# Optimization experiments

Measured on AMD Instinct MI355X. Metric: run time of the kernel, lower is better.

Reference implementation:

```python
import jax, jax.numpy as jnp
import numpy as np

B, C, N, D, F = 2048, 64, 64, 64, 128  # batch, cin_hidden, num_features, embed_dim, feature_maps


def setup_inputs() -> dict:
    key = jax.random.key(0)
    k1, k2, k3 = jax.random.split(key, 3)
    xj = jax.random.normal(k1, (B, C, D), dtype=jnp.float32)
    x0 = jax.random.normal(k2, (B, N, D), dtype=jnp.float32)
    # xavier_uniform_ on (F, C, N): fan_in = C*N? torch treats dim1 as fan_in-ish;
    # exact init distribution is irrelevant for correctness testing, use scaled uniform.
    limit = float(np.sqrt(6.0 / (C + N)))
    W = jax.random.uniform(k3, (F, C, N), dtype=jnp.float32, minval=-limit, maxval=limit)
    return {"xj": xj, "x0": x0, "W": W}


def reference(xj, x0, W):
    # Original: hadamard[b,c,n,d] = x0[b,n,d]*xj[b,c,d];
    # out[b,f,c,d] = sum_n hadamard * W[f,c,n]; cin_out = sum_c out; cin_p_out = sum_d cin_out.
    # Fused: cin_out[b,f,d] = sum_{c,n} W[f,c,n] * xj[b,c,d] * x0[b,n,d]
    cin_out = jnp.einsum('bcd,bnd,fcn->bfd', xj, x0, W)  # (B, F, D)
    cin_p_out = jnp.sum(cin_out, axis=-1)  # (B, F)
    return (cin_out, cin_p_out)
```

## Files before the change

### kernel.cpp

```cpp
#include <hip/hip_runtime.h>


typedef _Float16 f16;
typedef __attribute__((ext_vector_type(8))) _Float16 half8;
typedef __attribute__((ext_vector_type(16))) float f32x16;
typedef __attribute__((ext_vector_type(4))) float f32x4;

#define GLOAD16(g, l) __builtin_amdgcn_global_load_lds( \
    (const __attribute__((address_space(1))) void*)(g), \
    (__attribute__((address_space(3))) void*)(l), 16, 0, 0)

__global__ __launch_bounds__(256) void wconv_kernel(const float* __restrict__ W,
                                                    f16* __restrict__ Wh) {
  int i = (blockIdx.x * 256 + threadIdx.x) * 8;
  const float4 a = *(const float4*)(W + i);
  const float4 b = *(const float4*)(W + i + 4);
  half8 r;
  r[0] = (f16)a.x; r[1] = (f16)a.y; r[2] = (f16)a.z; r[3] = (f16)a.w;
  r[4] = (f16)b.x; r[5] = (f16)b.y; r[6] = (f16)b.z; r[7] = (f16)b.w;
  *(half8*)(Wh + i) = r;
}

__global__ __launch_bounds__(512, 2) void cin_kernel(
    const float* __restrict__ xj, const float* __restrict__ x0,
    const f16* __restrict__ Wh, float* __restrict__ out,
    float* __restrict__ pout) {
  __shared__ f16 x0T[4 * 4096];
  __shared__ f16 Wt[2 * 8192];

  const int t = threadIdx.x;
  const int wid = t >> 6, lane = t & 63;
  const int b0 = blockIdx.x * 4;

#pragma unroll
  for (int p = 0; p < 2; ++p) {
    const int s = p * 512 + wid * 64 + lane;
    const int f = s >> 3, ch = s & 7;
    const f16* gp = Wh + (size_t)f * 4096 + ((ch ^ (f & 7)) << 3);
    f16* lp = Wt + (p * 512 + wid * 64) * 8;
    GLOAD16(gp, lp);
  }

#pragma unroll
  for (int bb = 0; bb < 4; ++bb) {
    const float* s0 = x0 + (size_t)(b0 + bb) * 4096;
    const int n = lane, d0 = wid * 8;
    const float4 va = *(const float4*)(s0 + n * 64 + d0);
    const float4 vb = *(const float4*)(s0 + n * 64 + d0 + 4);
    const int chb = n >> 3, sub = n & 7;
#pragma unroll
    for (int j = 0; j < 8; ++j) {
      const float v = (j < 4) ? ((const float*)&va)[j] : ((const float*)&vb)[j - 4];
      const int d = d0 + j;
      x0T[bb * 4096 + d * 64 + ((chb ^ (d & 7)) << 3) + sub] = (f16)v;
    }
  }
  __syncthreads();

  const int wc = wid & 1, bb = wid >> 1;
  const int lr = lane & 31, hi = lane >> 5;

  half8 af[2][4];
#pragma unroll
  for (int mf = 0; mf < 2; ++mf) {
    const int d = mf * 32 + lr;
#pragma unroll
    for (int kk = 0; kk < 4; ++kk)
      af[mf][kk] = *(const half8*)&x0T[bb * 4096 + d * 64 +
                                       (((kk * 2 + hi) ^ (d & 7)) << 3)];
  }

  f32x16 acc[2][2] = {};

  const float* xjg = xj + (size_t)(b0 + bb) * 4096 + lr;
  float xjc0 = xjg[0], xjc1 = xjg[32];

  for (int c = 0; c < 64; ++c) {
    const int buf = c & 1;
    if (c < 63) {
#pragma unroll
      for (int p = 0; p < 2; ++p) {
        const int s = p * 512 + wid * 64 + lane;
        const int f = s >> 3, ch = s & 7;
        const f16* gp = Wh + (size_t)f * 4096 + (c + 1) * 64 + ((ch ^ (f & 7)) << 3);
        f16* lp = Wt + (buf ^ 1) * 8192 + (p * 512 + wid * 64) * 8;
        GLOAD16(gp, lp);
      }
    }
    float xjn0 = 0.f, xjn1 = 0.f;
    if (c < 63) { xjn0 = xjg[(c + 1) * 64]; xjn1 = xjg[(c + 1) * 64 + 32]; }

    half8 bf[2][4];
#pragma unroll
    for (int nf = 0; nf < 2; ++nf) {
      const int f = wc * 64 + nf * 32 + lr;
#pragma unroll
      for (int kk = 0; kk < 4; ++kk)
        bf[nf][kk] = *(const half8*)&Wt[buf * 8192 + f * 64 +
                                        (((kk * 2 + hi) ^ (f & 7)) << 3)];
    }

    const f16 xh0 = (f16)xjc0, xh1 = (f16)xjc1;
#pragma unroll
    for (int kk = 0; kk < 4; ++kk) {
      const half8 ap0 = af[0][kk] * xh0;
      const half8 ap1 = af[1][kk] * xh1;
      acc[0][0] = __builtin_amdgcn_mfma_f32_32x32x16_f16(ap0, bf[0][kk], acc[0][0], 0, 0, 0);
      acc[0][1] = __builtin_amdgcn_mfma_f32_32x32x16_f16(ap0, bf[1][kk], acc[0][1], 0, 0, 0);
      acc[1][0] = __builtin_amdgcn_mfma_f32_32x32x16_f16(ap1, bf[0][kk], acc[1][0], 0, 0, 0);
      acc[1][1] = __builtin_amdgcn_mfma_f32_32x32x16_f16(ap1, bf[1][kk], acc[1][1], 0, 0, 0);
    }
    xjc0 = xjn0; xjc1 = xjn1;
    __syncthreads();
  }

  const int b = b0 + bb;
  float* ob = out + (size_t)b * 8192;
  float psum[2] = {0.f, 0.f};
#pragma unroll
  for (int mf = 0; mf < 2; ++mf) {
#pragma unroll
    for (int nf = 0; nf < 2; ++nf) {
      const int f = wc * 64 + nf * 32 + lr;
      const f32x16 v = acc[mf][nf];
      float s = 0.f;
#pragma unroll
      for (int q = 0; q < 4; ++q) {
        f32x4 vv = { v[4 * q], v[4 * q + 1], v[4 * q + 2], v[4 * q + 3] };
        *(f32x4*)(ob + f * 64 + mf * 32 + q * 8 + hi * 4) = vv;
        s += vv[0] + vv[1] + vv[2] + vv[3];
      }
      psum[nf] += s;
    }
  }
#pragma unroll
  for (int nf = 0; nf < 2; ++nf) {
    float s = psum[nf];
    s += __shfl_xor(s, 32, 64);
    if (hi == 0) pout[(size_t)b * 128 + wc * 64 + nf * 32 + lr] = s;
  }
}

extern "C" void kernel_launch(void* const* d_in, const int* in_sizes, int n_in,
                              void* d_out, int out_size, void* d_ws, size_t ws_size,
                              hipStream_t stream) {
  const float* xj = (const float*)d_in[0];
  const float* x0 = (const float*)d_in[1];
  const float* W  = (const float*)d_in[2];
  float* out  = (float*)d_out;
  float* pout = out + (size_t)2048 * 128 * 64;
  f16* Wh = (f16*)d_ws;

  wconv_kernel<<<256, 256, 0, stream>>>(W, Wh);
  cin_kernel<<<512, 512, 0, stream>>>(xj, x0, Wh, out, pout);
}
```

Baseline: 153.4 us.

## Pre-scatter W into MFMA fragment layout and deepen W pipeline to four stages

The weight conversion kernel now writes W directly in per-channel MFMA B-fragment order. Each lane's B operand then comes from a contiguous LDS read with no swizzle arithmetic. The main loop keeps a 4-deep ring of W tiles in LDS, prefetched 3 channels ahead, and waits with an explicit vmcnt plus barrier instead of double buffering with a trailing __syncthreads. Waves are remapped so each one computes 32 features for two batches, with B fragments shared across four accumulators. This aims to hide global-load latency and cut LDS read cost, but doubles W LDS usage, which may reduce occupancy, and relies on a hand-counted vmcnt.

```diff
diff --git a/kernel.cpp b/kernel.cpp
--- a/kernel.cpp
+++ b/kernel.cpp
@@ -10,36 +10,32 @@
     (const __attribute__((address_space(1))) void*)(g), \
     (__attribute__((address_space(3))) void*)(l), 16, 0, 0)
 
-__global__ __launch_bounds__(256) void wconv_kernel(const float* __restrict__ W,
-                                                    f16* __restrict__ Wh) {
-  int i = (blockIdx.x * 256 + threadIdx.x) * 8;
-  const float4 a = *(const float4*)(W + i);
-  const float4 b = *(const float4*)(W + i + 4);
+__global__ __launch_bounds__(256) void wscat_kernel(const float* __restrict__ W,
+                                                    f16* __restrict__ Wb) {
+  const int tid = blockIdx.x * 256 + threadIdx.x;
+  const int c = tid >> 10, s = tid & 1023;
+  const int gk = s >> 6, ln = s & 63;
+  const int g = gk >> 2, kk = gk & 3, hi = ln >> 5, lr = ln & 31;
+  const int f = g * 32 + lr, n0 = kk * 16 + hi * 8;
+  const float* src = W + (size_t)f * 4096 + c * 64 + n0;
+  const float4 a = *(const float4*)src;
+  const float4 b = *(const float4*)(src + 4);
   half8 r;
   r[0] = (f16)a.x; r[1] = (f16)a.y; r[2] = (f16)a.z; r[3] = (f16)a.w;
   r[4] = (f16)b.x; r[5] = (f16)b.y; r[6] = (f16)b.z; r[7] = (f16)b.w;
-  *(half8*)(Wh + i) = r;
+  *(half8*)(Wb + (size_t)c * 8192 + s * 8) = r;
 }
 
 __global__ __launch_bounds__(512, 2) void cin_kernel(
     const float* __restrict__ xj, const float* __restrict__ x0,
-    const f16* __restrict__ Wh, float* __restrict__ out,
+    const f16* __restrict__ Wb, float* __restrict__ out,
     float* __restrict__ pout) {
   __shared__ f16 x0T[4 * 4096];
-  __shared__ f16 Wt[2 * 8192];
+  __shared__ f16 Wt[4 * 8192];
 
   const int t = threadIdx.x;
   const int wid = t >> 6, lane = t & 63;
   const int b0 = blockIdx.x * 4;
-
-#pragma unroll
-  for (int p = 0; p < 2; ++p) {
-    const int s = p * 512 + wid * 64 + lane;
-    const int f = s >> 3, ch = s & 7;
-    const f16* gp = Wh + (size_t)f * 4096 + ((ch ^ (f & 7)) << 3);
-    f16* lp = Wt + (p * 512 + wid * 64) * 8;
-    GLOAD16(gp, lp);
-  }
 
 #pragma unroll
   for (int bb = 0; bb < 4; ++bb) {
@@ -52,92 +48,93 @@
     for (int j = 0; j < 8; ++j) {
       const float v = (j < 4) ? ((const float*)&va)[j] : ((const float*)&vb)[j - 4];
       const int d = d0 + j;
-      x0T[bb * 4096 + d * 64 + ((chb ^ (d & 7)) << 3) + sub] = (f16)v;
+      x0T[bb * 4096 + d * 64 + (((chb) ^ (d & 7)) << 3) + sub] = (f16)v;
     }
   }
   __syncthreads();
 
-  const int wc = wid & 1, bb = wid >> 1;
+  const int wg = wid & 3, bp = wid >> 2;
   const int lr = lane & 31, hi = lane >> 5;
 
-  half8 af[2][4];
+  half8 af[4][4];
 #pragma unroll
-  for (int mf = 0; mf < 2; ++mf) {
-    const int d = mf * 32 + lr;
+  for (int mf = 0; mf < 4; ++mf) {
+    const int bb = bp * 2 + (mf >> 1);
+    const int d = (mf & 1) * 32 + lr;
 #pragma unroll
     for (int kk = 0; kk < 4; ++kk)
       af[mf][kk] = *(const half8*)&x0T[bb * 4096 + d * 64 +
                                        (((kk * 2 + hi) ^ (d & 7)) << 3)];
   }
 
-  f32x16 acc[2][2] = {};
+  f32x16 acc[4] = {};
 
-  const float* xjg = xj + (size_t)(b0 + bb) * 4096 + lr;
-  float xjc0 = xjg[0], xjc1 = xjg[32];
+  const f16* wsrc = Wb + ((size_t)wid * 64 + lane) * 8;
+  f16* wdst = Wt + ((size_t)wid * 64 + lane) * 8;
+  const float* xjp = xj + (size_t)(b0 + bp * 2) * 4096 + lr;
 
+#pragma unroll
+  for (int cc = 0; cc < 3; ++cc) {
+    GLOAD16(wsrc + (size_t)cc * 8192, wdst + cc * 8192);
+    GLOAD16(wsrc + (size_t)cc * 8192 + 4096, wdst + cc * 8192 + 4096);
+  }
+  float xc0 = xjp[0], xc1 = xjp[32], xc2 = xjp[4096], xc3 = xjp[4096 + 32];
+
+#pragma unroll 1
   for (int c = 0; c < 64; ++c) {
-    const int buf = c & 1;
-    if (c < 63) {
-#pragma unroll
-      for (int p = 0; p < 2; ++p) {
-        const int s = p * 512 + wid * 64 + lane;
-        const int f = s >> 3, ch = s & 7;
-        const f16* gp = Wh + (size_t)f * 4096 + (c + 1) * 64 + ((ch ^ (f & 7)) << 3);
-        f16* lp = Wt + (buf ^ 1) * 8192 + (p * 512 + wid * 64) * 8;
-        GLOAD16(gp, lp);
-      }
-    }
-    float xjn0 = 0.f, xjn1 = 0.f;
-    if (c < 63) { xjn0 = xjg[(c + 1) * 64]; xjn1 = xjg[(c + 1) * 64 + 32]; }
+    asm volatile("s_waitcnt vmcnt(8)" ::: "memory");
+    __builtin_amdgcn_s_barrier();
+    __builtin_amdgcn_sched_barrier(0);
 
-    half8 bf[2][4];
-#pragma unroll
-    for (int nf = 0; nf < 2; ++nf) {
-      const int f = wc * 64 + nf * 32 + lr;
-#pragma unroll
-      for (int kk = 0; kk < 4; ++kk)
-        bf[nf][kk] = *(const half8*)&Wt[buf * 8192 + f * 64 +
-                                        (((kk * 2 + hi) ^ (f & 7)) << 3)];
-    }
+    const f16* wb = Wt + (c & 3) * 8192 + wg * 2048;
+    half8 bf0 = *(const half8*)&wb[0 * 512 + lane * 8];
+    half8 bf1 = *(const half8*)&wb[1 * 512 + lane * 8];
+    half8 bf2 = *(const half8*)&wb[2 * 512 + lane * 8];
+    half8 bf3 = *(const half8*)&wb[3 * 512 + lane * 8];
 
-    const f16 xh0 = (f16)xjc0, xh1 = (f16)xjc1;
+    const int cs = (c < 61) ? c + 3 : 63;
+    GLOAD16(wsrc + (size_t)cs * 8192, wdst + ((c + 3) & 3) * 8192);
+    GLOAD16(wsrc + (size_t)cs * 8192 + 4096, wdst + ((c + 3) & 3) * 8192 + 4096);
+
+    const int cx = (c < 63) ? c + 1 : 63;
+    const float xn0 = xjp[cx * 64], xn1 = xjp[cx * 64 + 32];
+    const float xn2 = xjp[4096 + cx * 64], xn3 = xjp[4096 + cx * 64 + 32];
+
+    const f16 xh0 = (f16)xc0, xh1 = (f16)xc1, xh2 = (f16)xc2, xh3 = (f16)xc3;
 #pragma unroll
     for (int kk = 0; kk < 4; ++kk) {
-      const half8 ap0 = af[0][kk] * xh0;
-      const half8 ap1 = af[1][kk] * xh1;
-      acc[0][0] = __builtin_amdgcn_mfma_f32_32x32x16_f16(ap0, bf[0][kk], acc[0][0], 0, 0, 0);
-      acc[0][1] = __builtin_amdgcn_mfma_f32_32x32x16_f16(ap0, bf[1][kk], acc[0][1], 0, 0, 0);
-      acc[1][0] = __builtin_amdgcn_mfma_f32_32x32x16_f16(ap1, bf[0][kk], acc[1][0], 0, 0, 0);
-      acc[1][1] = __builtin_amdgcn_mfma_f32_32x32x16_f16(ap1, bf[1][kk], acc[1][1], 0, 0, 0);
+      const half8 bfv = (kk == 0) ? bf0 : (kk == 1) ? bf1 : (kk == 2) ? bf2 : bf3;
+      acc[0] = __builtin_amdgcn_mfma_f32_32x32x16_f16(af[0][kk] * xh0, bfv, acc[0], 0, 0, 0);
+      acc[1] = __builtin_amdgcn_mfma_f32_32x32x16_f16(af[1][kk] * xh1, bfv, acc[1], 0, 0, 0);
+      acc[2] = __builtin_amdgcn_mfma_f32_32x32x16_f16(af[2][kk] * xh2, bfv, acc[2], 0, 0, 0);
+      acc[3] = __builtin_amdgcn_mfma_f32_32x32x16_f16(af[3][kk] * xh3, bfv, acc[3], 0, 0, 0);
     }
-    xjc0 = xjn0; xjc1 = xjn1;
-    __syncthreads();
+    xc0 = xn0; xc1 = xn1; xc2 = xn2; xc3 = xn3;
   }
 
-  const int b = b0 + bb;
-  float* ob = out + (size_t)b * 8192;
-  float psum[2] = {0.f, 0.f};
+  const int fcol = wg * 32 + lr;
+  float ps[4];
 #pragma unroll
-  for (int mf = 0; mf < 2; ++mf) {
+  for (int mf = 0; mf < 4; ++mf) {
+    const int b = b0 + bp * 2 + (mf >> 1);
+    float* ob = out + (size_t)b * 8192 + (size_t)fcol * 64 + (mf & 1) * 32;
+    const f32x16 v = acc[mf];
+    float s = 0.f;
 #pragma unroll
-    for (int nf = 0; nf < 2; ++nf) {
-      const int f = wc * 64 + nf * 32 + lr;
-      const f32x16 v = acc[mf][nf];
-      float s = 0.f;
-#pragma unroll
-      for (int q = 0; q < 4; ++q) {
-        f32x4 vv = { v[4 * q], v[4 * q + 1], v[4 * q + 2], v[4 * q + 3] };
-        *(f32x4*)(ob + f * 64 + mf * 32 + q * 8 + hi * 4) = vv;
-        s += vv[0] + vv[1] + vv[2] + vv[3];
-      }
-      psum[nf] += s;
+    for (int q = 0; q < 4; ++q) {
+      f32x4 vv = { v[4 * q], v[4 * q + 1], v[4 * q + 2], v[4 * q + 3] };
+      *(f32x4*)(ob + q * 8 + hi * 4) = vv;
+      s += vv[0] + vv[1] + vv[2] + vv[3];
     }
+    ps[mf] = s;
   }
-#pragma unroll
-  for (int nf = 0; nf < 2; ++nf) {
-    float s = psum[nf];
-    s += __shfl_xor(s, 32, 64);
-    if (hi == 0) pout[(size_t)b * 128 + wc * 64 + nf * 32 + lr] = s;
+  float pA = ps[0] + ps[1];
+  float pB = ps[2] + ps[3];
+  pA += __shfl_xor(pA, 32, 64);
+  pB += __shfl_xor(pB, 32, 64);
+  if (hi == 0) {
+    pout[(size_t)(b0 + bp * 2) * 128 + fcol] = pA;
+    pout[(size_t)(b0 + bp * 2 + 1) * 128 + fcol] = pB;
   }
 }
 
@@ -149,8 +146,8 @@
   const float* W  = (const float*)d_in[2];
   float* out  = (float*)d_out;
   float* pout = out + (size_t)2048 * 128 * 64;
-  f16* Wh = (f16*)d_ws;
+  f16* Wb = (f16*)d_ws;
 
-  wconv_kernel<<<256, 256, 0, stream>>>(W, Wh);
-  cin_kernel<<<512, 512, 0, stream>>>(xj, x0, Wh, out, pout);
+  wscat_kernel<<<256, 256, 0, stream>>>(W, Wb);
+  cin_kernel<<<512, 512, 0, stream>>>(xj, x0, Wb, out, pout);
 }
```

Result: faster. 146.1 us (-4.8%).
